# Performance work log

Hardware: AMD Instinct MI355X
Metric: run time of the kernel (lower is better)

Reference implementation:

```python
import jax, jax.numpy as jnp
import numpy as np

D_MODEL = 768
N_HEADS = 8
Q_RANK = 64
KV_RANK = 64
ROPE_DIM = 64
NOPE_DIM = D_MODEL // N_HEADS - ROPE_DIM  # 32
V_DIM = D_MODEL // N_HEADS               # 96
Q_HEAD_DIM = NOPE_DIM + ROPE_DIM         # 96
EPS = 1e-6
ROPE_BASE = 10000.0


def rms_norm(x, w, eps=EPS):
    v = jnp.mean(jnp.square(x.astype(jnp.float32)), axis=-1, keepdims=True)
    return (x.astype(jnp.float32) * jax.lax.rsqrt(v + eps)).astype(x.dtype) * w


def rope_cos_sin(seq_len, dim):
    inv_freq = 1.0 / (ROPE_BASE ** (jnp.arange(0, dim, 2, dtype=jnp.float32) / dim))
    freqs = jnp.outer(jnp.arange(seq_len, dtype=jnp.float32), inv_freq)
    emb = jnp.concatenate([freqs, freqs], axis=-1)  # [s, dim]
    return jnp.cos(emb), jnp.sin(emb)


def apply_rope(x, cos, sin, pos_ids):
    # x: [b,h,s,d]; DeepSeek-V2 de-interleaves pairs before rotate_half
    b, h, s, d = x.shape
    x = x.reshape(b, h, s, d // 2, 2).transpose(0, 1, 2, 4, 3).reshape(b, h, s, d)
    c = cos[pos_ids][:, None]  # [b,1,s,d]
    sn = sin[pos_ids][:, None]
    x1, x2 = jnp.split(x, 2, axis=-1)
    rot = jnp.concatenate([-x2, x1], axis=-1)
    return x * c + rot * sn


def setup_inputs() -> dict:
    key = jax.random.key(0)
    ks = jax.random.split(key, 8)
    s = 0.02
    return {
        "src": jax.random.normal(ks[0], (4, 2048, D_MODEL), jnp.float32),
        "wq_a": jax.random.normal(ks[1], (Q_RANK, D_MODEL), jnp.float32) * s,
        "q_a_ln_w": jnp.ones((Q_RANK,), jnp.float32),
        "wq_b": jax.random.normal(ks[2], (N_HEADS * Q_HEAD_DIM, Q_RANK), jnp.float32) * s,
        "wkv_a": jax.random.normal(ks[3], (KV_RANK + ROPE_DIM, D_MODEL), jnp.float32) * s,
        "kv_a_ln_w": jnp.ones((KV_RANK,), jnp.float32),
        "wkv_b": jax.random.normal(ks[4], (N_HEADS * (NOPE_DIM + V_DIM), KV_RANK), jnp.float32) * s,
        "wo": jax.random.normal(ks[5], (D_MODEL, N_HEADS * V_DIM), jnp.float32) * s,
        "norm_w": jnp.ones((D_MODEL,), jnp.float32),
    }


def reference(src, wq_a, q_a_ln_w, wq_b, wkv_a, kv_a_ln_w, wkv_b, wo, norm_w):
    b, s, _ = src.shape
    pos = jnp.broadcast_to(jnp.arange(s)[None], (b, s))
    cos, sin = rope_cos_sin(s, ROPE_DIM)

    # ---- compress_kv (torch.no_grad in original) ----
    ckv = src @ wkv_a.T                                  # [b,s,rank+rope]
    c_lat, k_pe = ckv[..., :KV_RANK], ckv[..., KV_RANK:]
    c_lat = rms_norm(c_lat, kv_a_ln_w)
    k_pe = apply_rope(k_pe[:, None], cos, sin, pos)[:, 0]  # [b,s,rope]
    c_lat = jax.lax.stop_gradient(c_lat)
    k_pe = jax.lax.stop_gradient(k_pe)

    # ---- query path ----
    q = rms_norm(src @ wq_a.T, q_a_ln_w) @ wq_b.T        # [b,s,h*96]
    q = q.reshape(b, s, N_HEADS, Q_HEAD_DIM).transpose(0, 2, 1, 3)
    q_nope, q_pe = q[..., :NOPE_DIM], q[..., NOPE_DIM:]
    q_pe = apply_rope(q_pe, cos, sin, pos)

    # ---- absorb kv_b_proj ----
    w = wkv_b.reshape(N_HEADS, NOPE_DIM + V_DIM, KV_RANK)
    q_absorb, out_absorb = w[:, :NOPE_DIM], w[:, NOPE_DIM:]   # [h,32,r], [h,96,r]
    q_lat = jnp.einsum('bhsd,hdr->bhsr', q_nope, q_absorb)    # [b,h,s,r]

    scale = Q_HEAD_DIM ** -0.5
    scores = (jnp.einsum('bhsr,btr->bhst', q_lat, c_lat)
              + jnp.einsum('bhsd,btd->bhst', q_pe, k_pe)) * scale
    attn = jax.nn.softmax(scores.astype(jnp.float32), axis=-1).astype(src.dtype)

    ctx = jnp.einsum('bhst,btr->bhsr', attn, c_lat)           # [b,h,s,r]
    ctx = jnp.einsum('bhsr,hvr->bhsv', ctx, out_absorb)       # [b,h,s,96]
    attn_out = ctx.transpose(0, 2, 1, 3).reshape(b, s, N_HEADS * V_DIM) @ wo.T

    # residual (dropout in eval = identity) + RMSNorm
    return rms_norm(src + attn_out, norm_w)
```

## Files before the change

kernel.cpp:

```cpp
#include <hip/hip_runtime.h>


#define DEV static __device__ __forceinline__
typedef unsigned short ushort_t;
typedef __attribute__((ext_vector_type(8))) short bf8_t;
typedef __attribute__((ext_vector_type(4))) float f4_t;

DEV float bf2f(unsigned int u) {
    union { float f; unsigned int i; } x; x.i = u << 16; return x.f;
}
DEV ushort_t f2bf(float f) {
    union { float f; unsigned int u; } x; x.f = f;
    unsigned int u = x.u;
    return (ushort_t)((u + 0x7fffu + ((u >> 16) & 1u)) >> 16);
}
DEV float ldin(const void* p, size_t i, int isbf) {
    return isbf ? bf2f(((const ushort_t*)p)[i]) : ((const float*)p)[i];
}
DEV float fexp2(float x) {
#if __has_builtin(__builtin_amdgcn_exp2f)
    return __builtin_amdgcn_exp2f(x);
#else
    return exp2f(x);
#endif
}
DEV int get_isbf(const void* nw) {
    return ((((const unsigned int*)nw)[0] & 0xffffu) != 0u) ? 1 : 0;
}

constexpr int   TOK   = 4 * 2048;
constexpr float EPSF  = 1e-6f;
constexpr float QSCALE = (float)(0.10206207261596575 * 1.4426950408889634);
constexpr float L2_10000_OVER_32 = 0.4152410118609203f;

constexpr size_t OFF_WOT   = 0;
constexpr size_t OFF_WKVAT = 589824;
constexpr size_t OFF_WQAT  = 688128;
constexpr size_t OFF_WQBT  = 737280;
constexpr size_t OFF_QAF   = 786432;
constexpr size_t OFF_OAT   = 802816;
constexpr size_t OFF_QLN   = 851968;
constexpr size_t OFF_KVLN  = 852032;
constexpr size_t OFF_NW    = 852096;
constexpr size_t OFF_FLAG  = 852864;
constexpr size_t OFF_CTXF  = 852880;
constexpr size_t OFF_SRCBF = 3998608;
constexpr size_t OFF_KBF   = 7144336;
constexpr size_t OFF_VTB   = 7668624;
constexpr size_t OFF_QBF   = 7930768;
constexpr size_t OFF_ROPE  = 12125072;

constexpr int PB0 = 2304;
constexpr int PB1 = PB0 + 384;
constexpr int PB2 = PB1 + 192;
constexpr int PB3 = PB2 + 192;
constexpr int PB4 = PB3 + 64;
constexpr int PB5 = PB4 + 192;
constexpr int PB6 = PB5 + 4;
constexpr int PB7 = PB6 + 256;

__global__ __launch_bounds__(256) void prep_k(
    const void* __restrict__ wq_a, const void* __restrict__ q_ln,
    const void* __restrict__ wq_b, const void* __restrict__ wkv_a,
    const void* __restrict__ kv_ln, const void* __restrict__ wkv_b,
    const void* __restrict__ wo, const void* __restrict__ nw,
    float* __restrict__ ws)
{
    const int isbf = get_isbf(nw);
    const int bid = blockIdx.x;
    const int tid = threadIdx.x;
    if (bid < PB0) {
        int i = bid * 256 + tid;
        ushort_t* wob = (ushort_t*)(ws + OFF_WOT);
        wob[i] = isbf ? ((const ushort_t*)wo)[i] : f2bf(((const float*)wo)[i]);
    } else if (bid < PB1) {
        int i = (bid - PB0) * 256 + tid;
        ushort_t* d = (ushort_t*)(ws + OFF_WKVAT);
        d[i] = isbf ? ((const ushort_t*)wkv_a)[i] : f2bf(((const float*)wkv_a)[i]);
    } else if (bid < PB2) {
        int i = (bid - PB1) * 256 + tid;
        ushort_t* d = (ushort_t*)(ws + OFF_WQAT);
        d[i] = isbf ? ((const ushort_t*)wq_a)[i] : f2bf(((const float*)wq_a)[i]);
    } else if (bid < PB3) {
        int i = (bid - PB2) * 256 + tid;
        ushort_t* d = (ushort_t*)(ws + OFF_WQBT);
        d[i] = isbf ? ((const ushort_t*)wq_b)[i] : f2bf(((const float*)wq_b)[i]);
    } else if (bid < PB4) {
        int i = (bid - PB3) * 256 + tid;
        int h = i >> 11, rem = i & 2047, r = rem >> 5, d = rem & 31;
        ushort_t* dst = (ushort_t*)(ws + OFF_QAF);
        dst[i] = f2bf(ldin(wkv_b, (size_t)(h * 128 + d) * 64 + r, isbf) * QSCALE);
    } else if (bid < PB5) {
        int i = (bid - PB4) * 256 + tid;
        int h = i / 6144, rem = i - h * 6144;
        int r = rem / 96, v = rem - r * 96;
        ws[OFF_OAT + i] = ldin(wkv_b, (size_t)h * 8192 + 2048 + v * 64 + r, isbf);
    } else if (bid < PB6) {
        int i = (bid - PB5) * 256 + tid;
        if (i < 64)             ws[OFF_QLN + i]       = ldin(q_ln, i, isbf);
        else if (i < 128)       ws[OFF_KVLN + i - 64] = ldin(kv_ln, i - 64, isbf);
        else if (i < 128 + 768) ws[OFF_NW + i - 128]  = ldin(nw, i - 128, isbf);
    } else {
        int i = (bid - PB6) * 256 + tid;
        int pos = i >> 5, p = i & 31;
        float inv = exp2f(-(float)p * L2_10000_OVER_32);
        float ang = (float)pos * inv;
        float2* tab = (float2*)(ws + OFF_ROPE);
        tab[i] = make_float2(cosf(ang), sinf(ang));
    }
}

__global__ __launch_bounds__(512) void k1_ckv(
    const void* __restrict__ src, const void* __restrict__ nw,
    const float* __restrict__ ws,
    ushort_t* __restrict__ Kbf, ushort_t* __restrict__ VTbf,
    ushort_t* __restrict__ srcbf)
{
    const ushort_t* wkvab = (const ushort_t*)(ws + OFF_WKVAT);
    const float* kvln  = ws + OFF_KVLN;
    const float2* tab  = (const float2*)(ws + OFF_ROPE);
    const int isbf = get_isbf(nw);
    __shared__ __align__(16) ushort_t sA[32 * 776];
    __shared__ float ckv[32][132];
    int j = threadIdx.x;
    int t0 = blockIdx.x * 32;
    int w = j >> 6, lane = j & 63;
    int tl = lane & 15, qd = lane >> 4;

    {
        for (int e = j; e < 32 * 96; e += 512) {
            int row = e / 96, c8 = e - row * 96;
            size_t off = (size_t)(t0 + row) * 768 + c8 * 8;
            if (isbf) {
                uint4 v = *(const uint4*)((const ushort_t*)src + off);
                *(uint4*)(sA + row * 776 + c8 * 8) = v;
            } else {
                const float4* p = (const float4*)((const float*)src + off);
                float4 f0 = p[0], f1 = p[1];
                ushort_t tmp[8] = {f2bf(f0.x), f2bf(f0.y), f2bf(f0.z), f2bf(f0.w),
                                   f2bf(f1.x), f2bf(f1.y), f2bf(f1.z), f2bf(f1.w)};
                uint4 v = *(const uint4*)tmp;
                *(uint4*)(sA + row * 776 + c8 * 8) = v;
                *(uint4*)(srcbf + off) = v;
            }
        }
    }
    __syncthreads();
    {
        f4_t acc[2];
        acc[0] = (f4_t){0.f, 0.f, 0.f, 0.f};
        acc[1] = (f4_t){0.f, 0.f, 0.f, 0.f};
        const ushort_t* bp = wkvab + (size_t)(w * 16 + tl) * 768 + qd * 8;
#pragma unroll 4
        for (int ks = 0; ks < 24; ++ks) {
            bf8_t b  = *(const bf8_t*)(bp + ks * 32);
            bf8_t a0 = *(const bf8_t*)(sA + tl * 776 + ks * 32 + qd * 8);
            bf8_t a1 = *(const bf8_t*)(sA + (16 + tl) * 776 + ks * 32 + qd * 8);
            acc[0] = __builtin_amdgcn_mfma_f32_16x16x32_bf16(a0, b, acc[0], 0, 0, 0);
            acc[1] = __builtin_amdgcn_mfma_f32_16x16x32_bf16(a1, b, acc[1], 0, 0, 0);
        }
#pragma unroll
        for (int mt = 0; mt < 2; ++mt)
#pragma unroll
            for (int r = 0; r < 4; ++r)
                ckv[mt * 16 + qd * 4 + r][w * 16 + tl] = acc[mt][r];
    }
    __syncthreads();

    if (j < 256) {
        int tt = j >> 3, l = j & 7;
        float ss = 0.f;
#pragma unroll
        for (int i = 0; i < 8; ++i) { float v = ckv[tt][l * 8 + i]; ss += v * v; }
        ss += __shfl_xor(ss, 1); ss += __shfl_xor(ss, 2); ss += __shfl_xor(ss, 4);
        float rs = rsqrtf(ss * (1.f / 64.f) + EPSF);
        size_t base = (size_t)(t0 + tt) * 128;
        ushort_t kb[8];
        float clw[8];
#pragma unroll
        for (int i = 0; i < 8; ++i) {
            int o2 = l * 8 + i;
            float cl = ckv[tt][o2] * rs;
            if (isbf) cl = bf2f(f2bf(cl));
            clw[i] = cl * kvln[o2];
            kb[i] = f2bf(clw[i]);
        }
        uint4 pack;
        pack.x = kb[0] | ((unsigned)kb[1] << 16); pack.y = kb[2] | ((unsigned)kb[3] << 16);
        pack.z = kb[4] | ((unsigned)kb[5] << 16); pack.w = kb[6] | ((unsigned)kb[7] << 16);
        *(uint4*)&Kbf[base + l * 8] = pack;
        int pos = (t0 + tt) & 2047;
        ushort_t r0[4], r1[4];
#pragma unroll
        for (int i = 0; i < 4; ++i) {
            int p = l * 4 + i;
            float2 cssn = tab[pos * 32 + p];
            float e = ckv[tt][64 + 2 * p], od = ckv[tt][64 + 2 * p + 1];
            r0[i] = f2bf(e * cssn.x - od * cssn.y);
            r1[i] = f2bf(od * cssn.x + e * cssn.y);
        }
        uint2 p0, p1;
        p0.x = r0[0] | ((unsigned)r0[1] << 16); p0.y = r0[2] | ((unsigned)r0[3] << 16);
        p1.x = r1[0] | ((unsigned)r1[1] << 16); p1.y = r1[2] | ((unsigned)r1[3] << 16);
        *(uint2*)&Kbf[base + 64 + l * 4] = p0;
        *(uint2*)&Kbf[base + 96 + l * 4] = p1;
#pragma unroll
        for (int i = 0; i < 8; ++i) ckv[tt][l * 8 + i] = clw[i];
    }
    __syncthreads();
    if (j < 256) {
        int t = j & 31, rb = (j >> 5) * 8;
        int bb = t0 >> 11, col = (t0 & 2047) + t;
#pragma unroll
        for (int i = 0; i < 8; ++i) {
            int r = rb + i;
            VTbf[((size_t)(bb * 64 + r)) * 2048 + col] = f2bf(ckv[t][r]);
        }
    }
}

__global__ __launch_bounds__(128) void k2_q(
    const void* __restrict__ src, const void* __restrict__ nw,
    const float* __restrict__ ws, ushort_t* __restrict__ Qbf)
{
    const int isbf = get_isbf(nw);
    const ushort_t* srcb = isbf ? (const ushort_t*)src : (const ushort_t*)(ws + OFF_SRCBF);
    const ushort_t* wqab = (const ushort_t*)(ws + OFF_WQAT);
    const ushort_t* wqbb = (const ushort_t*)(ws + OFF_WQBT);
    const ushort_t* qabs = (const ushort_t*)(ws + OFF_QAF);
    const float2*   tab  = (const float2*)(ws + OFF_ROPE);
    const float*    qln  = ws + OFF_QLN;

    __shared__ __align__(16) ushort_t LDS[2 * 3968];
    int j = threadIdx.x;
    int w = j >> 6, lane = j & 63;
    int tl = lane & 15, qd = lane >> 4;
    ushort_t* tmpn = LDS + w * 3968;
    ushort_t* qn   = tmpn + 1152;
    ushort_t* qf   = qn + 640;
    int tokw = blockIdx.x * 16;

    f4_t C1[4];
#pragma unroll
    for (int nt = 0; nt < 4; ++nt) C1[nt] = (f4_t){0.f, 0.f, 0.f, 0.f};
    {
        const ushort_t* ap = srcb + (size_t)(tokw + tl) * 768 + qd * 8;
#pragma unroll 4
        for (int ks = 0; ks < 24; ++ks) {
            bf8_t a = *(const bf8_t*)(ap + ks * 32);
#pragma unroll
            for (int nt = 0; nt < 4; ++nt) {
                bf8_t bfr = *(const bf8_t*)(wqab + (size_t)(nt * 16 + tl) * 768 + ks * 32 + qd * 8);
                C1[nt] = __builtin_amdgcn_mfma_f32_16x16x32_bf16(a, bfr, C1[nt], 0, 0, 0);
            }
        }
    }
    float rsv[4];
#pragma unroll
    for (int r = 0; r < 4; ++r) {
        float s = C1[0][r] * C1[0][r] + C1[1][r] * C1[1][r]
                + C1[2][r] * C1[2][r] + C1[3][r] * C1[3][r];
        s += __shfl_xor(s, 1); s += __shfl_xor(s, 2);
        s += __shfl_xor(s, 4); s += __shfl_xor(s, 8);
        rsv[r] = rsqrtf(s * (1.f / 64.f) + EPSF);
    }
    float qlnv[4];
#pragma unroll
    for (int nt = 0; nt < 4; ++nt) qlnv[nt] = qln[nt * 16 + tl];
#pragma unroll
    for (int nt = 0; nt < 4; ++nt)
#pragma unroll
        for (int r = 0; r < 4; ++r) {
            float v = C1[nt][r] * rsv[r];
            if (isbf) v = bf2f(f2bf(v));
            tmpn[(qd * 4 + r) * 72 + nt * 16 + tl] = f2bf(v * qlnv[nt]);
        }
    bf8_t A2[2];
#pragma unroll
    for (int ks = 0; ks < 2; ++ks) A2[ks] = *(const bf8_t*)(tmpn + tl * 72 + ks * 32 + qd * 8);

    float csv[4][4], snv[4][4];
#pragma unroll
    for (int nt2 = 0; nt2 < 4; ++nt2) {
        int p = (nt2 * 16 + tl) >> 1;
#pragma unroll
        for (int r = 0; r < 4; ++r) {
            int pos = (tokw + qd * 4 + r) & 2047;
            float2 t = tab[pos * 32 + p];
            csv[nt2][r] = t.x * QSCALE;
            snv[nt2][r] = t.y * QSCALE;
        }
    }
    const bool evn = !(tl & 1);
    int bb = tokw >> 11, pos0 = tokw & 2047;

    for (int h = w * 4; h < w * 4 + 4; ++h) {
        f4_t C2[6];
#pragma unroll
        for (int nt = 0; nt < 6; ++nt) C2[nt] = (f4_t){0.f, 0.f, 0.f, 0.f};
#pragma unroll
        for (int nt = 0; nt < 6; ++nt)
#pragma unroll
            for (int ks = 0; ks < 2; ++ks) {
                bf8_t bfr = *(const bf8_t*)(wqbb + (size_t)(h * 96 + nt * 16 + tl) * 64 + ks * 32 + qd * 8);
                C2[nt] = __builtin_amdgcn_mfma_f32_16x16x32_bf16(A2[ks], bfr, C2[nt], 0, 0, 0);
            }
#pragma unroll
        for (int nt = 0; nt < 2; ++nt)
#pragma unroll
            for (int r = 0; r < 4; ++r)
                qn[(qd * 4 + r) * 40 + nt * 16 + tl] = f2bf(C2[nt][r]);
        bf8_t an = *(const bf8_t*)(qn + tl * 40 + qd * 8);
        f4_t C3[4];
#pragma unroll
        for (int nt = 0; nt < 4; ++nt) C3[nt] = (f4_t){0.f, 0.f, 0.f, 0.f};
#pragma unroll
        for (int nt = 0; nt < 4; ++nt) {
            bf8_t bfr = *(const bf8_t*)(qabs + (size_t)h * 2048 + (nt * 16 + tl) * 32 + qd * 8);
            C3[nt] = __builtin_amdgcn_mfma_f32_16x16x32_bf16(an, bfr, C3[nt], 0, 0, 0);
        }
#pragma unroll
        for (int nt = 0; nt < 4; ++nt)
#pragma unroll
            for (int r = 0; r < 4; ++r)
                qf[(qd * 4 + r) * 136 + nt * 16 + tl] = f2bf(C3[nt][r]);
#pragma unroll
        for (int nt2 = 0; nt2 < 4; ++nt2) {
            int p = (nt2 * 16 + tl) >> 1;
            int outc = evn ? (64 + p) : (96 + p);
#pragma unroll
            for (int r = 0; r < 4; ++r) {
                float val = C2[nt2 + 2][r];
                float part = __shfl_xor(val, 1);
                float res = evn ? (val * csv[nt2][r] - part * snv[nt2][r])
                                : (val * csv[nt2][r] + part * snv[nt2][r]);
                qf[(qd * 4 + r) * 136 + outc] = f2bf(res);
            }
        }
        size_t qb = ((size_t)(bb * 8 + h) * 2048 + pos0) * 128;
#pragma unroll
        for (int i = 0; i < 4; ++i) {
            int idx = i * 64 + lane;
            int row = idx >> 4, c = idx & 15;
            uint4 v = *(const uint4*)(qf + row * 136 + c * 8);
            *(uint4*)(Qbf + qb + (size_t)row * 128 + c * 8) = v;
        }
    }
}

__global__ __launch_bounds__(256, 2) void k3_attn(
    const ushort_t* __restrict__ Qbf, const ushort_t* __restrict__ Kbf,
    const ushort_t* __restrict__ VTbf, const float* __restrict__ oaT,
    ushort_t* __restrict__ ctxb)
{
    __shared__ __align__(16) ushort_t LDS[22528];
    ushort_t* Kt = LDS;
    ushort_t* Vt = LDS + 8704;
    ushort_t* Pw = LDS + 13312;
    int j = threadIdx.x;
    int b = blockIdx.z, h = blockIdx.y, q0g = blockIdx.x * 128;
    int w = j >> 6, lane = j & 63;
    int tl = lane & 15, qd = lane >> 4;
    ushort_t* Pme = Pw + w * 2304;
    int qw = q0g + w * 32;

    bf8_t qfA[4], qfB[4];
    {
        const ushort_t* qp = Qbf + ((size_t)((b * 8 + h) * 2048) + qw + tl) * 128 + qd * 8;
#pragma unroll
        for (int ks = 0; ks < 4; ++ks) {
            qfA[ks] = *(const bf8_t*)(qp + ks * 32);
            qfB[ks] = *(const bf8_t*)(qp + 16 * 128 + ks * 32);
        }
    }
    f4_t OaccA[4], OaccB[4];
#pragma unroll
    for (int nt = 0; nt < 4; ++nt) {
        OaccA[nt] = (f4_t){0.f, 0.f, 0.f, 0.f};
        OaccB[nt] = (f4_t){0.f, 0.f, 0.f, 0.f};
    }
    float lA = 0.f, lB = 0.f;

    const size_t kbase = (size_t)b * 2048 * 128;
    const size_t vbase = (size_t)b * 64 * 2048;

    for (int it = 0; it < 32; ++it) {
        __syncthreads();
        {
            int r = j >> 2, c0 = (j & 3) * 32;
            const uint4* gp = (const uint4*)(Kbf + kbase + (size_t)(it * 64 + r) * 128 + c0);
            uint4 a0 = gp[0], a1 = gp[1], a2 = gp[2], a3 = gp[3];
            uint4* dp = (uint4*)(Kt + r * 136 + c0);
            dp[0] = a0; dp[1] = a1; dp[2] = a2; dp[3] = a3;
        }
        {
            int d = j >> 2, c0 = (j & 3) * 16;
            const uint4* gp = (const uint4*)(VTbf + vbase + (size_t)d * 2048 + it * 64 + c0);
            uint4 a0 = gp[0], a1 = gp[1];
            uint4* dp = (uint4*)(Vt + d * 72 + c0);
            dp[0] = a0; dp[1] = a1;
        }
        __syncthreads();
        f4_t SA[4], SB[4];
        __builtin_amdgcn_s_setprio(1);
#pragma unroll
        for (int nt = 0; nt < 4; ++nt) {
            f4_t cA = (f4_t){0.f, 0.f, 0.f, 0.f};
            f4_t cB = (f4_t){0.f, 0.f, 0.f, 0.f};
#pragma unroll
            for (int ks = 0; ks < 4; ++ks) {
                bf8_t kf = *(const bf8_t*)(Kt + (nt * 16 + tl) * 136 + ks * 32 + qd * 8);
                cA = __builtin_amdgcn_mfma_f32_16x16x32_bf16(kf, qfA[ks], cA, 0, 0, 0);
                cB = __builtin_amdgcn_mfma_f32_16x16x32_bf16(kf, qfB[ks], cB, 0, 0, 0);
            }
            SA[nt] = cA; SB[nt] = cB;
        }
        __builtin_amdgcn_s_setprio(0);
        float rsA = 0.f, rsB = 0.f;
#pragma unroll
        for (int nt = 0; nt < 4; ++nt)
#pragma unroll
            for (int r = 0; r < 4; ++r) {
                float pA = fexp2(SA[nt][r]); SA[nt][r] = pA; rsA += pA;
                float pB = fexp2(SB[nt][r]); SB[nt][r] = pB; rsB += pB;
            }
        rsA += __shfl_xor(rsA, 16); rsA += __shfl_xor(rsA, 32);
        rsB += __shfl_xor(rsB, 16); rsB += __shfl_xor(rsB, 32);
        lA += rsA; lB += rsB;
#pragma unroll
        for (int nt = 0; nt < 4; ++nt) {
            uint2 pkA, pkB;
            pkA.x = f2bf(SA[nt][0]) | ((unsigned)f2bf(SA[nt][1]) << 16);
            pkA.y = f2bf(SA[nt][2]) | ((unsigned)f2bf(SA[nt][3]) << 16);
            pkB.x = f2bf(SB[nt][0]) | ((unsigned)f2bf(SB[nt][1]) << 16);
            pkB.y = f2bf(SB[nt][2]) | ((unsigned)f2bf(SB[nt][3]) << 16);
            *(uint2*)(Pme + tl * 72 + nt * 16 + qd * 4) = pkA;
            *(uint2*)(Pme + (16 + tl) * 72 + nt * 16 + qd * 4) = pkB;
        }
        bf8_t pfA[2], pfB[2];
#pragma unroll
        for (int ks = 0; ks < 2; ++ks) {
            pfA[ks] = *(const bf8_t*)(Pme + tl * 72 + ks * 32 + qd * 8);
            pfB[ks] = *(const bf8_t*)(Pme + (16 + tl) * 72 + ks * 32 + qd * 8);
        }
        __builtin_amdgcn_s_setprio(1);
#pragma unroll
        for (int nt = 0; nt < 4; ++nt)
#pragma unroll
            for (int ks = 0; ks < 2; ++ks) {
                bf8_t vf = *(const bf8_t*)(Vt + (nt * 16 + tl) * 72 + ks * 32 + qd * 8);
                OaccA[nt] = __builtin_amdgcn_mfma_f32_16x16x32_bf16(pfA[ks], vf, OaccA[nt], 0, 0, 0);
                OaccB[nt] = __builtin_amdgcn_mfma_f32_16x16x32_bf16(pfB[ks], vf, OaccB[nt], 0, 0, 0);
            }
        __builtin_amdgcn_s_setprio(0);
    }
    {
        float linvA[4], linvB[4];
#pragma unroll
        for (int r = 0; r < 4; ++r) {
            float lqA = __shfl(lA, (lane & 48) + qd * 4 + r);
            float lqB = __shfl(lB, (lane & 48) + qd * 4 + r);
            linvA[r] = 1.f / lqA; linvB[r] = 1.f / lqB;
        }
#pragma unroll
        for (int nt = 0; nt < 4; ++nt)
#pragma unroll
            for (int r = 0; r < 4; ++r) {
                Pme[(qd * 4 + r) * 72 + nt * 16 + tl] = f2bf(OaccA[nt][r] * linvA[r]);
                Pme[(16 + qd * 4 + r) * 72 + nt * 16 + tl] = f2bf(OaccB[nt][r] * linvB[r]);
            }
    }
    __syncthreads();
    ushort_t* OA = LDS;
    for (int e = j; e < 96 * 64; e += 256) {
        int v = e >> 6, r = e & 63;
        OA[v * 72 + r] = f2bf(oaT[h * 6144 + r * 96 + v]);
    }
    __syncthreads();
    {
        bf8_t ofA[2], ofB[2];
#pragma unroll
        for (int ks = 0; ks < 2; ++ks) {
            ofA[ks] = *(const bf8_t*)(Pme + tl * 72 + ks * 32 + qd * 8);
            ofB[ks] = *(const bf8_t*)(Pme + (16 + tl) * 72 + ks * 32 + qd * 8);
        }
        __builtin_amdgcn_s_setprio(1);
#pragma unroll
        for (int nt = 0; nt < 6; ++nt) {
            f4_t cA = (f4_t){0.f, 0.f, 0.f, 0.f};
            f4_t cB = (f4_t){0.f, 0.f, 0.f, 0.f};
#pragma unroll
            for (int ks = 0; ks < 2; ++ks) {
                bf8_t af = *(const bf8_t*)(OA + (nt * 16 + tl) * 72 + ks * 32 + qd * 8);
                cA = __builtin_amdgcn_mfma_f32_16x16x32_bf16(ofA[ks], af, cA, 0, 0, 0);
                cB = __builtin_amdgcn_mfma_f32_16x16x32_bf16(ofB[ks], af, cB, 0, 0, 0);
            }
#pragma unroll
            for (int r = 0; r < 4; ++r) {
                size_t tokA = (size_t)(b * 2048 + qw + qd * 4 + r);
                size_t tokB = tokA + 16;
                ctxb[tokA * 768 + h * 96 + nt * 16 + tl] = f2bf(cA[r]);
                ctxb[tokB * 768 + h * 96 + nt * 16 + tl] = f2bf(cB[r]);
            }
        }
        __builtin_amdgcn_s_setprio(0);
    }
}

__global__ __launch_bounds__(512, 2) void k5a_gemm(
    const void* __restrict__ src, const void* __restrict__ nw,
    const float* __restrict__ ws,
    const ushort_t* __restrict__ ctxb, ushort_t* __restrict__ ybf)
{
    const ushort_t* woB = (const ushort_t*)(ws + OFF_WOT);
    const int isbf = get_isbf(nw);
    __shared__ __align__(16) ushort_t sB[384 * 72];
    __shared__ __align__(16) ushort_t sA[32 * 72];
    int j = threadIdx.x;
    int bx = blockIdx.x;
    int t0 = (bx >> 1) * 32;
    int colh = (bx & 1) * 384;
    int w = j >> 6, lane = j & 63;
    int tl = lane & 15, qd = lane >> 4;
    int mt = w & 1;
    int n0l = (w >> 1) * 96;

    f4_t acc[6];
#pragma unroll
    for (int nt = 0; nt < 6; ++nt) acc[nt] = (f4_t){0.f, 0.f, 0.f, 0.f};

    for (int kb = 0; kb < 12; ++kb) {
        __syncthreads();
        {
            for (int e = j; e < 384 * 8; e += 512) {
                int rr = e >> 3, ch = e & 7;
                uint4 v = *(const uint4*)(woB + (size_t)(colh + rr) * 768 + kb * 64 + ch * 8);
                *(uint4*)(sB + rr * 72 + ch * 8) = v;
            }
        }
        if (j < 256) {
            int rr = j >> 3, ch = j & 7;
            uint4 v = *(const uint4*)(ctxb + (size_t)(t0 + rr) * 768 + kb * 64 + ch * 8);
            *(uint4*)(sA + rr * 72 + ch * 8) = v;
        }
        __syncthreads();
        __builtin_amdgcn_s_setprio(1);
#pragma unroll
        for (int ks = 0; ks < 2; ++ks) {
            bf8_t a = *(const bf8_t*)(sA + (mt * 16 + tl) * 72 + ks * 32 + qd * 8);
#pragma unroll
            for (int nt = 0; nt < 6; ++nt) {
                bf8_t bfr = *(const bf8_t*)(sB + (n0l + nt * 16 + tl) * 72 + ks * 32 + qd * 8);
                acc[nt] = __builtin_amdgcn_mfma_f32_16x16x32_bf16(a, bfr, acc[nt], 0, 0, 0);
            }
        }
        __builtin_amdgcn_s_setprio(0);
    }
#pragma unroll
    for (int nt = 0; nt < 6; ++nt)
#pragma unroll
        for (int r = 0; r < 4; ++r) {
            int row = t0 + mt * 16 + qd * 4 + r;
            int col = colh + n0l + nt * 16 + tl;
            float yv = acc[nt][r] + ldin(src, (size_t)row * 768 + col, isbf);
            ybf[(size_t)row * 768 + col] = f2bf(yv);
        }
}

__global__ __launch_bounds__(256) void k5b_norm(
    const void* __restrict__ nw_in, const float* __restrict__ ws,
    const ushort_t* __restrict__ ybf, void* __restrict__ out)
{
    const float* nw = ws + OFF_NW;
    const int isbf = get_isbf(nw_in);
    int j = threadIdx.x;
    int tt = j >> 4, s = j & 15;
    size_t row = (size_t)blockIdx.x * 16 + tt;
    const ushort_t* yp = ybf + row * 768 + s * 48;

    float val[48];
    float ss = 0.f;
#pragma unroll
    for (int c8 = 0; c8 < 6; ++c8) {
        union { uint4 u; ushort_t h[8]; } uu;
        uu.u = ((const uint4*)yp)[c8];
#pragma unroll
        for (int c = 0; c < 8; ++c) {
            float v = bf2f(uu.h[c]);
            val[c8 * 8 + c] = v;
            ss += v * v;
        }
    }
    ss += __shfl_xor(ss, 1); ss += __shfl_xor(ss, 2);
    ss += __shfl_xor(ss, 4); ss += __shfl_xor(ss, 8);
    float rs = rsqrtf(ss * (1.f / 768.f) + EPSF);
    const float* nwp = nw + s * 48;
    size_t base = row * 768 + s * 48;
    if (isbf) {
        ushort_t* op = (ushort_t*)out + base;
#pragma unroll
        for (int c8 = 0; c8 < 6; ++c8) {
            union { uint4 u; ushort_t h[8]; } uu;
#pragma unroll
            for (int c = 0; c < 8; ++c) {
                float hv = bf2f(f2bf(val[c8 * 8 + c] * rs));
                uu.h[c] = f2bf(hv * nwp[c8 * 8 + c]);
            }
            ((uint4*)op)[c8] = uu.u;
        }
    } else {
        float* op = (float*)out + base;
#pragma unroll
        for (int c4 = 0; c4 < 12; ++c4) {
            float4 f;
            f.x = val[c4 * 4 + 0] * rs * nwp[c4 * 4 + 0];
            f.y = val[c4 * 4 + 1] * rs * nwp[c4 * 4 + 1];
            f.z = val[c4 * 4 + 2] * rs * nwp[c4 * 4 + 2];
            f.w = val[c4 * 4 + 3] * rs * nwp[c4 * 4 + 3];
            ((float4*)op)[c4] = f;
        }
    }
}

extern "C" void kernel_launch(void* const* d_in, const int* in_sizes, int n_in,
                              void* d_out, int out_size, void* d_ws, size_t ws_size,
                              hipStream_t stream)
{
    const void* src   = d_in[0];
    const void* wq_a  = d_in[1];
    const void* q_ln  = d_in[2];
    const void* wq_b  = d_in[3];
    const void* wkv_a = d_in[4];
    const void* kv_ln = d_in[5];
    const void* wkv_b = d_in[6];
    const void* wo    = d_in[7];
    const void* nw    = d_in[8];
    float* ws = (float*)d_ws;
    ushort_t* Kbf   = (ushort_t*)(ws + OFF_KBF);
    ushort_t* VTbf  = (ushort_t*)(ws + OFF_VTB);
    ushort_t* Qbf   = (ushort_t*)(ws + OFF_QBF);
    ushort_t* ctxb  = (ushort_t*)(ws + OFF_CTXF);
    ushort_t* srcbf = (ushort_t*)(ws + OFF_SRCBF);
    ushort_t* ybf   = Qbf;

    prep_k<<<dim3(PB7), dim3(256), 0, stream>>>(wq_a, q_ln, wq_b, wkv_a, kv_ln, wkv_b, wo, nw, ws);
    k1_ckv<<<dim3(TOK / 32), dim3(512), 0, stream>>>(src, nw, ws, Kbf, VTbf, srcbf);
    k2_q<<<dim3(TOK / 16), dim3(128), 0, stream>>>(src, nw, ws, Qbf);
    k3_attn<<<dim3(16, 8, 4), dim3(256), 0, stream>>>(Qbf, Kbf, VTbf, ws + OFF_OAT, ctxb);
    k5a_gemm<<<dim3(TOK / 32 * 2), dim3(512), 0, stream>>>(src, nw, ws, ctxb, ybf);
    k5b_norm<<<dim3(TOK / 16), dim3(256), 0, stream>>>(nw, ws, ybf, d_out);
}
```

Before: 268.0 us.

## Split query projection into normalized-latent kernel and per-head LDS-staged q kernel

The query kernel is split in two. The first kernel computes the q_a projection and RMSNorm and writes the normalized 64-wide latent to a scratch buffer that reuses the ctx workspace. The second kernel stages half of wq_b into LDS and gives each wave a 16-token tile for a single head, instead of one wave looping over four heads. This aims to raise parallelism and cut repeated global reads of wq_b, at the cost of an extra launch and a round trip of the latent through global memory.

After: 260.5 us. -2.8%, faster.

```diff
diff --git a/kernel.cpp b/kernel.cpp
--- a/kernel.cpp
+++ b/kernel.cpp
@@ -219,25 +219,19 @@
     }
 }
 
-__global__ __launch_bounds__(128) void k2_q(
+__global__ __launch_bounds__(128) void k2a_qn(
     const void* __restrict__ src, const void* __restrict__ nw,
-    const float* __restrict__ ws, ushort_t* __restrict__ Qbf)
+    const float* __restrict__ ws, ushort_t* __restrict__ qn_all)
 {
     const int isbf = get_isbf(nw);
     const ushort_t* srcb = isbf ? (const ushort_t*)src : (const ushort_t*)(ws + OFF_SRCBF);
     const ushort_t* wqab = (const ushort_t*)(ws + OFF_WQAT);
-    const ushort_t* wqbb = (const ushort_t*)(ws + OFF_WQBT);
-    const ushort_t* qabs = (const ushort_t*)(ws + OFF_QAF);
-    const float2*   tab  = (const float2*)(ws + OFF_ROPE);
     const float*    qln  = ws + OFF_QLN;
-
-    __shared__ __align__(16) ushort_t LDS[2 * 3968];
+    __shared__ __align__(16) ushort_t LDS[2 * 1152];
     int j = threadIdx.x;
     int w = j >> 6, lane = j & 63;
     int tl = lane & 15, qd = lane >> 4;
-    ushort_t* tmpn = LDS + w * 3968;
-    ushort_t* qn   = tmpn + 1152;
-    ushort_t* qf   = qn + 640;
+    ushort_t* tmpn = LDS + w * 1152;
     int tokw = blockIdx.x * 16;
 
     f4_t C1[4];
@@ -275,9 +269,58 @@
             if (isbf) v = bf2f(f2bf(v));
             tmpn[(qd * 4 + r) * 72 + nt * 16 + tl] = f2bf(v * qlnv[nt]);
         }
+    if (w == 0) {
+#pragma unroll
+        for (int i = 0; i < 2; ++i) {
+            int e = i * 64 + lane;
+            int row = e >> 3, ch = e & 7;
+            uint4 v = *(const uint4*)(tmpn + row * 72 + ch * 8);
+            *(uint4*)(qn_all + (size_t)(tokw + row) * 64 + ch * 8) = v;
+        }
+    }
+}
+
+__global__ __launch_bounds__(512) void k2b_q(
+    const float* __restrict__ ws, const ushort_t* __restrict__ qn_all,
+    ushort_t* __restrict__ Qbf)
+{
+    const ushort_t* wqbb = (const ushort_t*)(ws + OFF_WQBT);
+    const ushort_t* qabs = (const ushort_t*)(ws + OFF_QAF);
+    const float2*   tab  = (const float2*)(ws + OFF_ROPE);
+
+    __shared__ __align__(16) ushort_t sB[384 * 72];
+    __shared__ __align__(16) ushort_t sA[32 * 72];
+    __shared__ __align__(16) ushort_t PW[8 * 2816];
+    int j = threadIdx.x;
+    int bx = blockIdx.x;
+    int t0 = (bx >> 1) * 32;
+    int colh = (bx & 1) * 384;
+    int w = j >> 6, lane = j & 63;
+    int tl = lane & 15, qd = lane >> 4;
+    int mt = w & 1, hh = w >> 1;
+    int h = (bx & 1) * 4 + hh;
+    ushort_t* qnb = PW + w * 2816;
+    ushort_t* qf  = qnb + 640;
+    int tokw = t0 + mt * 16;
+
+    {
+        for (int e = j; e < 384 * 8; e += 512) {
+            int rr = e >> 3, ch = e & 7;
+            uint4 v = *(const uint4*)(wqbb + (size_t)(colh + rr) * 64 + ch * 8);
+            *(uint4*)(sB + rr * 72 + ch * 8) = v;
+        }
+    }
+    if (j < 256) {
+        int rr = j >> 3, ch = j & 7;
+        uint4 v = *(const uint4*)(qn_all + (size_t)(t0 + rr) * 64 + ch * 8);
+        *(uint4*)(sA + rr * 72 + ch * 8) = v;
+    }
+    __syncthreads();
+
     bf8_t A2[2];
 #pragma unroll
-    for (int ks = 0; ks < 2; ++ks) A2[ks] = *(const bf8_t*)(tmpn + tl * 72 + ks * 32 + qd * 8);
+    for (int ks = 0; ks < 2; ++ks)
+        A2[ks] = *(const bf8_t*)(sA + (mt * 16 + tl) * 72 + ks * 32 + qd * 8);
 
     float csv[4][4], snv[4][4];
 #pragma unroll
@@ -294,57 +337,55 @@
     const bool evn = !(tl & 1);
     int bb = tokw >> 11, pos0 = tokw & 2047;
 
-    for (int h = w * 4; h < w * 4 + 4; ++h) {
-        f4_t C2[6];
-#pragma unroll
-        for (int nt = 0; nt < 6; ++nt) C2[nt] = (f4_t){0.f, 0.f, 0.f, 0.f};
-#pragma unroll
-        for (int nt = 0; nt < 6; ++nt)
-#pragma unroll
-            for (int ks = 0; ks < 2; ++ks) {
-                bf8_t bfr = *(const bf8_t*)(wqbb + (size_t)(h * 96 + nt * 16 + tl) * 64 + ks * 32 + qd * 8);
-                C2[nt] = __builtin_amdgcn_mfma_f32_16x16x32_bf16(A2[ks], bfr, C2[nt], 0, 0, 0);
-            }
-#pragma unroll
-        for (int nt = 0; nt < 2; ++nt)
-#pragma unroll
-            for (int r = 0; r < 4; ++r)
-                qn[(qd * 4 + r) * 40 + nt * 16 + tl] = f2bf(C2[nt][r]);
-        bf8_t an = *(const bf8_t*)(qn + tl * 40 + qd * 8);
-        f4_t C3[4];
-#pragma unroll
-        for (int nt = 0; nt < 4; ++nt) C3[nt] = (f4_t){0.f, 0.f, 0.f, 0.f};
-#pragma unroll
-        for (int nt = 0; nt < 4; ++nt) {
-            bf8_t bfr = *(const bf8_t*)(qabs + (size_t)h * 2048 + (nt * 16 + tl) * 32 + qd * 8);
-            C3[nt] = __builtin_amdgcn_mfma_f32_16x16x32_bf16(an, bfr, C3[nt], 0, 0, 0);
-        }
-#pragma unroll
-        for (int nt = 0; nt < 4; ++nt)
-#pragma unroll
-            for (int r = 0; r < 4; ++r)
-                qf[(qd * 4 + r) * 136 + nt * 16 + tl] = f2bf(C3[nt][r]);
-#pragma unroll
-        for (int nt2 = 0; nt2 < 4; ++nt2) {
-            int p = (nt2 * 16 + tl) >> 1;
-            int outc = evn ? (64 + p) : (96 + p);
-#pragma unroll
-            for (int r = 0; r < 4; ++r) {
-                float val = C2[nt2 + 2][r];
-                float part = __shfl_xor(val, 1);
-                float res = evn ? (val * csv[nt2][r] - part * snv[nt2][r])
-                                : (val * csv[nt2][r] + part * snv[nt2][r]);
-                qf[(qd * 4 + r) * 136 + outc] = f2bf(res);
-            }
-        }
-        size_t qb = ((size_t)(bb * 8 + h) * 2048 + pos0) * 128;
-#pragma unroll
-        for (int i = 0; i < 4; ++i) {
-            int idx = i * 64 + lane;
-            int row = idx >> 4, c = idx & 15;
-            uint4 v = *(const uint4*)(qf + row * 136 + c * 8);
-            *(uint4*)(Qbf + qb + (size_t)row * 128 + c * 8) = v;
-        }
+    f4_t C2[6];
+#pragma unroll
+    for (int nt = 0; nt < 6; ++nt) C2[nt] = (f4_t){0.f, 0.f, 0.f, 0.f};
+#pragma unroll
+    for (int nt = 0; nt < 6; ++nt)
+#pragma unroll
+        for (int ks = 0; ks < 2; ++ks) {
+            bf8_t bfr = *(const bf8_t*)(sB + (hh * 96 + nt * 16 + tl) * 72 + ks * 32 + qd * 8);
+            C2[nt] = __builtin_amdgcn_mfma_f32_16x16x32_bf16(A2[ks], bfr, C2[nt], 0, 0, 0);
+        }
+#pragma unroll
+    for (int nt = 0; nt < 2; ++nt)
+#pragma unroll
+        for (int r = 0; r < 4; ++r)
+            qnb[(qd * 4 + r) * 40 + nt * 16 + tl] = f2bf(C2[nt][r]);
+    bf8_t an = *(const bf8_t*)(qnb + tl * 40 + qd * 8);
+    f4_t C3[4];
+#pragma unroll
+    for (int nt = 0; nt < 4; ++nt) C3[nt] = (f4_t){0.f, 0.f, 0.f, 0.f};
+#pragma unroll
+    for (int nt = 0; nt < 4; ++nt) {
+        bf8_t bfr = *(const bf8_t*)(qabs + (size_t)h * 2048 + (nt * 16 + tl) * 32 + qd * 8);
+        C3[nt] = __builtin_amdgcn_mfma_f32_16x16x32_bf16(an, bfr, C3[nt], 0, 0, 0);
+    }
+#pragma unroll
+    for (int nt = 0; nt < 4; ++nt)
+#pragma unroll
+        for (int r = 0; r < 4; ++r)
+            qf[(qd * 4 + r) * 136 + nt * 16 + tl] = f2bf(C3[nt][r]);
+#pragma unroll
+    for (int nt2 = 0; nt2 < 4; ++nt2) {
+        int p = (nt2 * 16 + tl) >> 1;
+        int outc = evn ? (64 + p) : (96 + p);
+#pragma unroll
+        for (int r = 0; r < 4; ++r) {
+            float val = C2[nt2 + 2][r];
+            float part = __shfl_xor(val, 1);
+            float res = evn ? (val * csv[nt2][r] - part * snv[nt2][r])
+                            : (val * csv[nt2][r] + part * snv[nt2][r]);
+            qf[(qd * 4 + r) * 136 + outc] = f2bf(res);
+        }
+    }
+    size_t qb = ((size_t)(bb * 8 + h) * 2048 + pos0) * 128;
+#pragma unroll
+    for (int i = 0; i < 4; ++i) {
+        int idx = i * 64 + lane;
+        int row = idx >> 4, c = idx & 15;
+        uint4 v = *(const uint4*)(qf + row * 136 + c * 8);
+        *(uint4*)(Qbf + qb + (size_t)row * 128 + c * 8) = v;
     }
 }
 
@@ -642,10 +683,12 @@
     ushort_t* ctxb  = (ushort_t*)(ws + OFF_CTXF);
     ushort_t* srcbf = (ushort_t*)(ws + OFF_SRCBF);
     ushort_t* ybf   = Qbf;
+    ushort_t* qn    = ctxb;
 
     prep_k<<<dim3(PB7), dim3(256), 0, stream>>>(wq_a, q_ln, wq_b, wkv_a, kv_ln, wkv_b, wo, nw, ws);
     k1_ckv<<<dim3(TOK / 32), dim3(512), 0, stream>>>(src, nw, ws, Kbf, VTbf, srcbf);
-    k2_q<<<dim3(TOK / 16), dim3(128), 0, stream>>>(src, nw, ws, Qbf);
+    k2a_qn<<<dim3(TOK / 16), dim3(128), 0, stream>>>(src, nw, ws, qn);
+    k2b_q<<<dim3(TOK / 32 * 2), dim3(512), 0, stream>>>(ws, qn, Qbf);
     k3_attn<<<dim3(16, 8, 4), dim3(256), 0, stream>>>(Qbf, Kbf, VTbf, ws + OFF_OAT, ctxb);
     k5a_gemm<<<dim3(TOK / 32 * 2), dim3(512), 0, stream>>>(src, nw, ws, ctxb, ybf);
     k5b_norm<<<dim3(TOK / 16), dim3(256), 0, stream>>>(nw, ws, ybf, d_out);
```
